# Optimization experiments

Measured on AMD Instinct MI355X. Metric: run time of the kernel, lower is better.

The kernel has to match this reference:

```python
import jax, jax.numpy as jnp
import numpy as np

ROUTING_ITERS = 3
EPS = 1e-8

def _squash_elem(s):
    # Faithful to torch squash with dim=-1 over a trailing size-1 axis: elementwise.
    sq = s * s
    return (sq / (1.0 + sq)) * s / jnp.sqrt(sq + EPS)

def setup_inputs() -> dict:
    key = jax.random.key(0)
    k1, k2 = jax.random.split(key)
    x = jax.random.normal(k1, (64, 1152, 64), dtype=jnp.float32)            # [B, N_routes, in_ch]
    route_weights = jax.random.normal(k2, (32, 1152, 64, 64), dtype=jnp.float32)  # [C, N, out, in]
    return {"x": x, "route_weights": route_weights}

def reference(x, route_weights):
    B = x.shape[0]
    C, N, O, _ = route_weights.shape
    # u_hat: [B, C, N, O]  (torch trailing size-1 dim dropped; squash/sums over it are elementwise)
    u_hat = jnp.einsum('cnoi,bni->bcno', route_weights, x)
    b_ij = jnp.zeros((B, C, N, 1), dtype=x.dtype)
    v_j = None
    for i in range(ROUTING_ITERS):
        c_ij = jax.nn.softmax(b_ij, axis=1)                  # over capsules
        s_j = jnp.sum(c_ij * u_hat, axis=2, keepdims=True)   # [B, C, 1, O]
        v_j = _squash_elem(s_j)
        if i < ROUTING_ITERS - 1:
            # torch: b_ij + (u_hat * v_j).sum(-1, keepdim) over size-1 dim -> broadcasts to [B,C,N,O]
            b_ij = b_ij + u_hat * v_j
    return v_j[:, :, 0, :]  # [B, C, O]
```

## Files before the change

### kernel.cpp

```cpp
#include <hip/hip_runtime.h>
#include <hip/hip_bf16.h>

typedef short short8v __attribute__((ext_vector_type(8)));
typedef float float4v __attribute__((ext_vector_type(4)));

constexpr int Bb = 64;
constexpr int Cc = 32;
constexpr int Nn = 1152;
constexpr int Oo = 64;
constexpr int Ii = 64;
constexpr int NCH = 32;
constexpr int CHN = 36;
constexpr int OT  = 16;
constexpr int COLS = 128;

__device__ __forceinline__ unsigned short bf16_rne(float f) {
    unsigned u = __float_as_uint(f);
    u += 0x7FFFu + ((u >> 16) & 1u);
    return (unsigned short)(u >> 16);
}
__device__ __forceinline__ float bf16_f(unsigned short h) {
    return __uint_as_float(((unsigned)h) << 16);
}
__device__ __forceinline__ float squash_elem(float s) {
    float sq = s * s;
    return (sq / (1.f + sq)) * s / sqrtf(sq + 1e-8f);
}

__global__ __launch_bounds__(256) void prep_x(const float* __restrict__ x,
                                              unsigned short* __restrict__ xh,
                                              unsigned short* __restrict__ xl) {
    size_t g = (size_t)blockIdx.x * 256 + threadIdx.x;
    float4 v = ((const float4*)x)[g];
    float a[4] = {v.x, v.y, v.z, v.w};
    ushort4 H, L;
    unsigned short* hp = (unsigned short*)&H;
    unsigned short* lp = (unsigned short*)&L;
#pragma unroll
    for (int e = 0; e < 4; ++e) {
        unsigned short hb = bf16_rne(a[e]);
        hp[e] = hb;
        lp[e] = bf16_rne(a[e] - bf16_f(hb));
    }
    ((ushort4*)xh)[g] = H;
    ((ushort4*)xl)[g] = L;
}

template <int MODE>
__global__ __launch_bounds__(256, 2) void caps_pass(
    const float* __restrict__ w, const unsigned short* __restrict__ xh,
    const unsigned short* __restrict__ xl, const float* __restrict__ V,
    float* __restrict__ part) {
    __shared__ unsigned short sh[2][COLS * 64];
    __shared__ unsigned short sl[2][COLS * 64];

    const int t = threadIdx.x;
    const int l = t & 63, wv = t >> 6;
    const int ch = blockIdx.x, ot = blockIdx.y;
    const int obase = ot * 4;
    const int kg = l >> 4;
    const int lm = l & 15;
    const int n0 = ch * CHN;
    const int sw = (lm & 7) << 3;

    float Vreg[8][4];
    if constexpr (MODE == 1) {
#pragma unroll
        for (int t8 = 0; t8 < 8; ++t8)
#pragma unroll
            for (int r = 0; r < 4; ++r) {
                int b = 16 * wv + 4 * kg + r;
                int c = 4 * t8 + ((l >> 2) & 3);
                int o = obase + (l & 3);
                Vreg[t8][r] = V[((size_t)b * Cc + c) * Oo + o];
            }
    }
    float4v acc4[8];
    float accs[8][4];
#pragma unroll
    for (int t8 = 0; t8 < 8; ++t8) {
        acc4[t8] = (float4v){0.f, 0.f, 0.f, 0.f};
#pragma unroll
        for (int r = 0; r < 4; ++r) accs[t8][r] = 0.f;
    }

    const int i0 = (t & 15) * 4;
    const int colb = t >> 4;
    float4 L0[8], L1[8];

    auto issue = [&](int n, float4(&ld)[8]) {
#pragma unroll
        for (int k = 0; k < 8; ++k) {
            int col = colb + 16 * k;
            int c = col >> 2, olc = col & 3;
            ld[k] = *(const float4*)(
                w + (((size_t)c * Nn + n) * Oo + obase + olc) * Ii + i0);
        }
    };
    auto writebuf = [&](unsigned short* dh, unsigned short* dl,
                        const float4(&ld)[8]) {
#pragma unroll
        for (int k = 0; k < 8; ++k) {
            int col = colb + 16 * k;
            int off = col * 64 + (i0 ^ ((col & 7) << 3));
            float a[4] = {ld[k].x, ld[k].y, ld[k].z, ld[k].w};
            ushort4 H, L;
            unsigned short* hp = (unsigned short*)&H;
            unsigned short* lp = (unsigned short*)&L;
#pragma unroll
            for (int e = 0; e < 4; ++e) {
                unsigned short hb = bf16_rne(a[e]);
                hp[e] = hb;
                lp[e] = bf16_rne(a[e] - bf16_f(hb));
            }
            *(ushort4*)(dh + off) = H;
            *(ushort4*)(dl + off) = L;
        }
    };
    auto compute = [&](const unsigned short* bh_, const unsigned short* bl_,
                       int n) {
        const size_t xoff = ((size_t)(16 * wv + lm) * Nn + n) * Ii + kg * 8;
        short8v ah0 = *(const short8v*)(xh + xoff);
        short8v al0 = *(const short8v*)(xl + xoff);
        short8v ah1 = *(const short8v*)(xh + xoff + 32);
        short8v al1 = *(const short8v*)(xl + xoff + 32);

        float u[8][4];
#pragma unroll
        for (int t8 = 0; t8 < 8; ++t8) {
            int row = 16 * t8 + lm;
            int c0 = row * 64 + ((kg * 8) ^ sw);
            int c1 = row * 64 + (((kg * 8) + 32) ^ sw);
            short8v bh0 = *(const short8v*)(bh_ + c0);
            short8v bl0 = *(const short8v*)(bl_ + c0);
            short8v bh1 = *(const short8v*)(bh_ + c1);
            short8v bl1 = *(const short8v*)(bl_ + c1);
            float4v a;
            if constexpr (MODE == 0) a = acc4[t8];
            else a = (float4v){0.f, 0.f, 0.f, 0.f};
            a = __builtin_amdgcn_mfma_f32_16x16x32_bf16(ah0, bh0, a, 0, 0, 0);
            a = __builtin_amdgcn_mfma_f32_16x16x32_bf16(al0, bh0, a, 0, 0, 0);
            a = __builtin_amdgcn_mfma_f32_16x16x32_bf16(ah0, bl0, a, 0, 0, 0);
            a = __builtin_amdgcn_mfma_f32_16x16x32_bf16(ah1, bh1, a, 0, 0, 0);
            a = __builtin_amdgcn_mfma_f32_16x16x32_bf16(al1, bh1, a, 0, 0, 0);
            a = __builtin_amdgcn_mfma_f32_16x16x32_bf16(ah1, bl1, a, 0, 0, 0);
            if constexpr (MODE == 0) {
                acc4[t8] = a;
            } else {
                u[t8][0] = a[0]; u[t8][1] = a[1];
                u[t8][2] = a[2]; u[t8][3] = a[3];
            }
        }
        if constexpr (MODE == 1) {
#pragma unroll
            for (int r = 0; r < 4; ++r) {
                float m = -1e30f;
#pragma unroll
                for (int t8 = 0; t8 < 8; ++t8)
                    m = fmaxf(m, u[t8][r] * Vreg[t8][r]);
                m = fmaxf(m, __shfl_xor(m, 4));
                m = fmaxf(m, __shfl_xor(m, 8));
                float Z = 0.f;
#pragma unroll
                for (int t8 = 0; t8 < 8; ++t8) {
                    float e = __expf(u[t8][r] * Vreg[t8][r] - m);
                    Z += e;
                    u[t8][r] *= e;
                }
                Z += __shfl_xor(Z, 4);
                Z += __shfl_xor(Z, 8);
                float rz = 1.f / Z;
#pragma unroll
                for (int t8 = 0; t8 < 8; ++t8) accs[t8][r] += u[t8][r] * rz;
            }
        }
    };

    issue(n0, L0);
    writebuf(sh[0], sl[0], L0);
    issue(n0 + 1, L1);
    __syncthreads();

    for (int j = 0; j < CHN; j += 2) {
        writebuf(sh[1], sl[1], L1);
        if (j + 2 < CHN) issue(n0 + j + 2, L0);
        compute(sh[0], sl[0], n0 + j);
        __syncthreads();
        if (j + 2 < CHN) writebuf(sh[0], sl[0], L0);
        if (j + 3 < CHN) issue(n0 + j + 3, L1);
        compute(sh[1], sl[1], n0 + j + 1);
        __syncthreads();
    }

#pragma unroll
    for (int t8 = 0; t8 < 8; ++t8)
#pragma unroll
        for (int r = 0; r < 4; ++r) {
            int b = 16 * wv + 4 * kg + r;
            int c = 4 * t8 + ((l >> 2) & 3);
            int o = obase + (l & 3);
            float val = (MODE == 0) ? acc4[t8][r] : accs[t8][r];
            part[(((size_t)ch * Bb + b) * Cc + c) * Oo + o] = val;
        }
}

__global__ void reduce_caps(const float* __restrict__ part,
                            float* __restrict__ V, float* __restrict__ out,
                            int mode) {
    int bc = blockIdx.x;
    int o = threadIdx.x;
    size_t base = (size_t)bc * 64 + o;
    float s = 0.f;
    for (int c = 0; c < NCH; ++c) s += part[(size_t)c * (Bb * Cc * Oo) + base];
    if (mode == 0)      V[base] = squash_elem(s * (1.f / 32.f));
    else if (mode == 1) V[base] += squash_elem(s);
    else                out[base] = squash_elem(s);
}

extern "C" void kernel_launch(void* const* d_in, const int* in_sizes, int n_in,
                              void* d_out, int out_size, void* d_ws, size_t ws_size,
                              hipStream_t stream) {
    const float* x = (const float*)d_in[0];
    const float* w = (const float*)d_in[1];
    float* out = (float*)d_out;

    const size_t XE = (size_t)Bb * Nn * Ii;
    unsigned short* xh = (unsigned short*)d_ws;
    unsigned short* xl = xh + XE;
    float* part = (float*)(xl + XE);
    float* V = part + (size_t)NCH * Bb * Cc * Oo;

    prep_x<<<(int)(XE / 4 / 256), 256, 0, stream>>>(x, xh, xl);

    caps_pass<0><<<dim3(NCH, OT), 256, 0, stream>>>(w, xh, xl, nullptr, part);
    reduce_caps<<<Bb * Cc, 64, 0, stream>>>(part, V, out, 0);
    caps_pass<1><<<dim3(NCH, OT), 256, 0, stream>>>(w, xh, xl, V, part);
    reduce_caps<<<Bb * Cc, 64, 0, stream>>>(part, V, out, 1);
    caps_pass<1><<<dim3(NCH, OT), 256, 0, stream>>>(w, xh, xl, V, part);
    reduce_caps<<<Bb * Cc, 64, 0, stream>>>(part, V, out, 2);
}
```

Baseline: 495.3 us.

## Load weights directly into MFMA registers, dropping LDS staging

The kernel no longer stages the weight tile through double-buffered shared memory. Each wave now reads its MFMA B-operand fragments straight from global memory and splits them into bf16 hi/lo in registers. The low part is now truncated instead of rounded. The chunk count rises from 32 to 48 and the occupancy hint from 2 to 3 blocks per SM, to hide latency through more parallelism. In exchange, each of the four waves now redundantly loads the same weights (relying on cache), there is no explicit software prefetch, and a bare s_barrier is kept per iteration.

```diff
diff --git a/kernel.cpp b/kernel.cpp
--- a/kernel.cpp
+++ b/kernel.cpp
@@ -9,10 +9,9 @@
 constexpr int Nn = 1152;
 constexpr int Oo = 64;
 constexpr int Ii = 64;
-constexpr int NCH = 32;
-constexpr int CHN = 36;
+constexpr int NCH = 48;
+constexpr int CHN = 24;
 constexpr int OT  = 16;
-constexpr int COLS = 128;
 
 __device__ __forceinline__ unsigned short bf16_rne(float f) {
     unsigned u = __float_as_uint(f);
@@ -25,6 +24,19 @@
 __device__ __forceinline__ float squash_elem(float s) {
     float sq = s * s;
     return (sq / (1.f + sq)) * s / sqrtf(sq + 1e-8f);
+}
+
+__device__ __forceinline__ void split8(const float4& f0, const float4& f1,
+                                       short8v& h, short8v& lo) {
+    float a[8] = {f0.x, f0.y, f0.z, f0.w, f1.x, f1.y, f1.z, f1.w};
+#pragma unroll
+    for (int e = 0; e < 8; ++e) {
+        unsigned b = __float_as_uint(a[e]);
+        unsigned r = b + 0x7FFFu + ((b >> 16) & 1u);
+        h[e] = (short)(r >> 16);
+        float res = a[e] - __uint_as_float(r & 0xFFFF0000u);
+        lo[e] = (short)(__float_as_uint(res) >> 16);
+    }
 }
 
 __global__ __launch_bounds__(256) void prep_x(const float* __restrict__ x,
@@ -47,33 +59,29 @@
 }
 
 template <int MODE>
-__global__ __launch_bounds__(256, 2) void caps_pass(
+__global__ __launch_bounds__(256, 3) void caps_pass(
     const float* __restrict__ w, const unsigned short* __restrict__ xh,
     const unsigned short* __restrict__ xl, const float* __restrict__ V,
     float* __restrict__ part) {
-    __shared__ unsigned short sh[2][COLS * 64];
-    __shared__ unsigned short sl[2][COLS * 64];
-
     const int t = threadIdx.x;
     const int l = t & 63, wv = t >> 6;
     const int ch = blockIdx.x, ot = blockIdx.y;
     const int obase = ot * 4;
-    const int kg = l >> 4;
-    const int lm = l & 15;
+    const int kg = l >> 4, lm = l & 15;
+    const int cc0 = lm >> 2, ol = lm & 3;
     const int n0 = ch * CHN;
-    const int sw = (lm & 7) << 3;
 
     float Vreg[8][4];
     if constexpr (MODE == 1) {
 #pragma unroll
-        for (int t8 = 0; t8 < 8; ++t8)
+        for (int t8 = 0; t8 < 8; ++t8) {
+            int c = 4 * t8 + cc0;
 #pragma unroll
             for (int r = 0; r < 4; ++r) {
                 int b = 16 * wv + 4 * kg + r;
-                int c = 4 * t8 + ((l >> 2) & 3);
-                int o = obase + (l & 3);
-                Vreg[t8][r] = V[((size_t)b * Cc + c) * Oo + o];
+                Vreg[t8][r] = V[((size_t)b * Cc + c) * Oo + obase + ol];
             }
+        }
     }
     float4v acc4[8];
     float accs[8][4];
@@ -84,57 +92,32 @@
         for (int r = 0; r < 4; ++r) accs[t8][r] = 0.f;
     }
 
-    const int i0 = (t & 15) * 4;
-    const int colb = t >> 4;
-    float4 L0[8], L1[8];
-
-    auto issue = [&](int n, float4(&ld)[8]) {
-#pragma unroll
-        for (int k = 0; k < 8; ++k) {
-            int col = colb + 16 * k;
-            int c = col >> 2, olc = col & 3;
-            ld[k] = *(const float4*)(
-                w + (((size_t)c * Nn + n) * Oo + obase + olc) * Ii + i0);
-        }
-    };
-    auto writebuf = [&](unsigned short* dh, unsigned short* dl,
-                        const float4(&ld)[8]) {
-#pragma unroll
-        for (int k = 0; k < 8; ++k) {
-            int col = colb + 16 * k;
-            int off = col * 64 + (i0 ^ ((col & 7) << 3));
-            float a[4] = {ld[k].x, ld[k].y, ld[k].z, ld[k].w};
-            ushort4 H, L;
-            unsigned short* hp = (unsigned short*)&H;
-            unsigned short* lp = (unsigned short*)&L;
-#pragma unroll
-            for (int e = 0; e < 4; ++e) {
-                unsigned short hb = bf16_rne(a[e]);
-                hp[e] = hb;
-                lp[e] = bf16_rne(a[e] - bf16_f(hb));
-            }
-            *(ushort4*)(dh + off) = H;
-            *(ushort4*)(dl + off) = L;
-        }
-    };
-    auto compute = [&](const unsigned short* bh_, const unsigned short* bl_,
-                       int n) {
-        const size_t xoff = ((size_t)(16 * wv + lm) * Nn + n) * Ii + kg * 8;
-        short8v ah0 = *(const short8v*)(xh + xoff);
-        short8v al0 = *(const short8v*)(xl + xoff);
-        short8v ah1 = *(const short8v*)(xh + xoff + 32);
-        short8v al1 = *(const short8v*)(xl + xoff + 32);
+    const size_t wlane = ((size_t)cc0 * Nn * Oo + obase + ol) * Ii + kg * 8;
+    const size_t xlane = (size_t)(16 * wv + lm) * Nn * Ii + kg * 8;
+    constexpr size_t T8STRIDE = (size_t)4 * Nn * Oo * Ii;
+
+    for (int j = 0; j < CHN; ++j) {
+        const int n = n0 + j;
+        const float* wn = w + wlane + (size_t)n * (Oo * Ii);
+        const unsigned short* xhn = xh + xlane + (size_t)n * Ii;
+        const unsigned short* xln = xl + xlane + (size_t)n * Ii;
+
+        short8v ah0 = *(const short8v*)xhn;
+        short8v al0 = *(const short8v*)xln;
+        short8v ah1 = *(const short8v*)(xhn + 32);
+        short8v al1 = *(const short8v*)(xln + 32);
 
         float u[8][4];
 #pragma unroll
         for (int t8 = 0; t8 < 8; ++t8) {
-            int row = 16 * t8 + lm;
-            int c0 = row * 64 + ((kg * 8) ^ sw);
-            int c1 = row * 64 + (((kg * 8) + 32) ^ sw);
-            short8v bh0 = *(const short8v*)(bh_ + c0);
-            short8v bl0 = *(const short8v*)(bl_ + c0);
-            short8v bh1 = *(const short8v*)(bh_ + c1);
-            short8v bl1 = *(const short8v*)(bl_ + c1);
+            const float* wp = wn + (size_t)t8 * T8STRIDE;
+            float4 f0 = *(const float4*)(wp);
+            float4 f1 = *(const float4*)(wp + 4);
+            float4 f2 = *(const float4*)(wp + 32);
+            float4 f3 = *(const float4*)(wp + 36);
+            short8v bh0, bl0, bh1, bl1;
+            split8(f0, f1, bh0, bl0);
+            split8(f2, f3, bh1, bl1);
             float4v a;
             if constexpr (MODE == 0) a = acc4[t8];
             else a = (float4v){0.f, 0.f, 0.f, 0.f};
@@ -151,6 +134,7 @@
                 u[t8][2] = a[2]; u[t8][3] = a[3];
             }
         }
+
         if constexpr (MODE == 1) {
 #pragma unroll
             for (int r = 0; r < 4; ++r) {
@@ -174,22 +158,8 @@
                 for (int t8 = 0; t8 < 8; ++t8) accs[t8][r] += u[t8][r] * rz;
             }
         }
-    };
-
-    issue(n0, L0);
-    writebuf(sh[0], sl[0], L0);
-    issue(n0 + 1, L1);
-    __syncthreads();
-
-    for (int j = 0; j < CHN; j += 2) {
-        writebuf(sh[1], sl[1], L1);
-        if (j + 2 < CHN) issue(n0 + j + 2, L0);
-        compute(sh[0], sl[0], n0 + j);
-        __syncthreads();
-        if (j + 2 < CHN) writebuf(sh[0], sl[0], L0);
-        if (j + 3 < CHN) issue(n0 + j + 3, L1);
-        compute(sh[1], sl[1], n0 + j + 1);
-        __syncthreads();
+
+        __builtin_amdgcn_s_barrier();
     }
 
 #pragma unroll
@@ -197,8 +167,8 @@
 #pragma unroll
         for (int r = 0; r < 4; ++r) {
             int b = 16 * wv + 4 * kg + r;
-            int c = 4 * t8 + ((l >> 2) & 3);
-            int o = obase + (l & 3);
+            int c = 4 * t8 + cc0;
+            int o = obase + ol;
             float val = (MODE == 0) ? acc4[t8][r] : accs[t8][r];
             part[(((size_t)ch * Bb + b) * Cc + c) * Oo + o] = val;
         }
```

Result: slower. 1.019 ms (+105.6%).

## Repartition MFMA work so each wave owns one output column across all batches

Applied to the files above, without the earlier changes.

Each wave now handles a single output index o across all 64 batch rows and 32 capsules. The old split gave each wave 16 batch rows across all 128 (c,o) columns. The LDS layout of the weight tile is reordered so a wave's 32 capsule rows are contiguous. Each wave then holds only 2 B-fragments in registers and streams x fragments for 4 batch quarters, double-buffered in registers. This cuts LDS reads of the weight tile per wave, but raises global/L2 reads of the bf16 x split by 4x per wave. In the routing pass the softmax over capsules now needs cross-lane shuffles over 16 lanes instead of mostly in-register reductions.

```diff
diff --git a/kernel.cpp b/kernel.cpp
--- a/kernel.cpp
+++ b/kernel.cpp
@@ -12,7 +12,6 @@
 constexpr int NCH = 32;
 constexpr int CHN = 36;
 constexpr int OT  = 16;
-constexpr int COLS = 128;
 
 __device__ __forceinline__ unsigned short bf16_rne(float f) {
     unsigned u = __float_as_uint(f);
@@ -51,38 +50,41 @@
     const float* __restrict__ w, const unsigned short* __restrict__ xh,
     const unsigned short* __restrict__ xl, const float* __restrict__ V,
     float* __restrict__ part) {
-    __shared__ unsigned short sh[2][COLS * 64];
-    __shared__ unsigned short sl[2][COLS * 64];
+    __shared__ unsigned short sh[2][128 * 64];
+    __shared__ unsigned short sl[2][128 * 64];
 
     const int t = threadIdx.x;
     const int l = t & 63, wv = t >> 6;
     const int ch = blockIdx.x, ot = blockIdx.y;
     const int obase = ot * 4;
-    const int kg = l >> 4;
-    const int lm = l & 15;
+    const int o = obase + wv;
+    const int kg = l >> 4, lm = l & 15;
     const int n0 = ch * CHN;
     const int sw = (lm & 7) << 3;
 
-    float Vreg[8][4];
+    float Vreg[4][2][4];
     if constexpr (MODE == 1) {
 #pragma unroll
-        for (int t8 = 0; t8 < 8; ++t8)
-#pragma unroll
-            for (int r = 0; r < 4; ++r) {
-                int b = 16 * wv + 4 * kg + r;
-                int c = 4 * t8 + ((l >> 2) & 3);
-                int o = obase + (l & 3);
-                Vreg[t8][r] = V[((size_t)b * Cc + c) * Oo + o];
-            }
+        for (int bq = 0; bq < 4; ++bq)
+#pragma unroll
+            for (int t8l = 0; t8l < 2; ++t8l)
+#pragma unroll
+                for (int r = 0; r < 4; ++r) {
+                    int b = 16 * bq + 4 * kg + r;
+                    int c = 16 * t8l + lm;
+                    Vreg[bq][t8l][r] = V[((size_t)b * Cc + c) * Oo + o];
+                }
     }
-    float4v acc4[8];
-    float accs[8][4];
-#pragma unroll
-    for (int t8 = 0; t8 < 8; ++t8) {
-        acc4[t8] = (float4v){0.f, 0.f, 0.f, 0.f};
-#pragma unroll
-        for (int r = 0; r < 4; ++r) accs[t8][r] = 0.f;
-    }
+    float4v acc4[4][2];
+    float accs[4][2][4];
+#pragma unroll
+    for (int bq = 0; bq < 4; ++bq)
+#pragma unroll
+        for (int t8l = 0; t8l < 2; ++t8l) {
+            acc4[bq][t8l] = (float4v){0.f, 0.f, 0.f, 0.f};
+#pragma unroll
+            for (int r = 0; r < 4; ++r) accs[bq][t8l][r] = 0.f;
+        }
 
     const int i0 = (t & 15) * 4;
     const int colb = t >> 4;
@@ -102,7 +104,9 @@
 #pragma unroll
         for (int k = 0; k < 8; ++k) {
             int col = colb + 16 * k;
-            int off = col * 64 + (i0 ^ ((col & 7) << 3));
+            int c = col >> 2, olc = col & 3;
+            int row = olc * 32 + c;
+            int off = row * 64 + (i0 ^ ((row & 7) << 3));
             float a[4] = {ld[k].x, ld[k].y, ld[k].z, ld[k].w};
             ushort4 H, L;
             unsigned short* hp = (unsigned short*)&H;
@@ -117,61 +121,79 @@
             *(ushort4*)(dl + off) = L;
         }
     };
+
     auto compute = [&](const unsigned short* bh_, const unsigned short* bl_,
                        int n) {
-        const size_t xoff = ((size_t)(16 * wv + lm) * Nn + n) * Ii + kg * 8;
-        short8v ah0 = *(const short8v*)(xh + xoff);
-        short8v al0 = *(const short8v*)(xl + xoff);
-        short8v ah1 = *(const short8v*)(xh + xoff + 32);
-        short8v al1 = *(const short8v*)(xl + xoff + 32);
-
-        float u[8][4];
-#pragma unroll
-        for (int t8 = 0; t8 < 8; ++t8) {
-            int row = 16 * t8 + lm;
+        short8v Bh0[2], Bl0[2], Bh1[2], Bl1[2];
+#pragma unroll
+        for (int t8l = 0; t8l < 2; ++t8l) {
+            int row = 32 * wv + 16 * t8l + lm;
             int c0 = row * 64 + ((kg * 8) ^ sw);
             int c1 = row * 64 + (((kg * 8) + 32) ^ sw);
-            short8v bh0 = *(const short8v*)(bh_ + c0);
-            short8v bl0 = *(const short8v*)(bl_ + c0);
-            short8v bh1 = *(const short8v*)(bh_ + c1);
-            short8v bl1 = *(const short8v*)(bl_ + c1);
-            float4v a;
-            if constexpr (MODE == 0) a = acc4[t8];
-            else a = (float4v){0.f, 0.f, 0.f, 0.f};
-            a = __builtin_amdgcn_mfma_f32_16x16x32_bf16(ah0, bh0, a, 0, 0, 0);
-            a = __builtin_amdgcn_mfma_f32_16x16x32_bf16(al0, bh0, a, 0, 0, 0);
-            a = __builtin_amdgcn_mfma_f32_16x16x32_bf16(ah0, bl0, a, 0, 0, 0);
-            a = __builtin_amdgcn_mfma_f32_16x16x32_bf16(ah1, bh1, a, 0, 0, 0);
-            a = __builtin_amdgcn_mfma_f32_16x16x32_bf16(al1, bh1, a, 0, 0, 0);
-            a = __builtin_amdgcn_mfma_f32_16x16x32_bf16(ah1, bl1, a, 0, 0, 0);
-            if constexpr (MODE == 0) {
-                acc4[t8] = a;
-            } else {
-                u[t8][0] = a[0]; u[t8][1] = a[1];
-                u[t8][2] = a[2]; u[t8][3] = a[3];
-            }
-        }
-        if constexpr (MODE == 1) {
-#pragma unroll
-            for (int r = 0; r < 4; ++r) {
-                float m = -1e30f;
-#pragma unroll
-                for (int t8 = 0; t8 < 8; ++t8)
-                    m = fmaxf(m, u[t8][r] * Vreg[t8][r]);
-                m = fmaxf(m, __shfl_xor(m, 4));
-                m = fmaxf(m, __shfl_xor(m, 8));
-                float Z = 0.f;
-#pragma unroll
-                for (int t8 = 0; t8 < 8; ++t8) {
-                    float e = __expf(u[t8][r] * Vreg[t8][r] - m);
-                    Z += e;
-                    u[t8][r] *= e;
+            Bh0[t8l] = *(const short8v*)(bh_ + c0);
+            Bl0[t8l] = *(const short8v*)(bl_ + c0);
+            Bh1[t8l] = *(const short8v*)(bh_ + c1);
+            Bl1[t8l] = *(const short8v*)(bl_ + c1);
+        }
+        short8v Ah0[2], Al0[2], Ah1[2], Al1[2];
+        {
+            const size_t xo = ((size_t)lm * Nn + n) * Ii + kg * 8;
+            Ah0[0] = *(const short8v*)(xh + xo);
+            Al0[0] = *(const short8v*)(xl + xo);
+            Ah1[0] = *(const short8v*)(xh + xo + 32);
+            Al1[0] = *(const short8v*)(xl + xo + 32);
+        }
+#pragma unroll
+        for (int bq = 0; bq < 4; ++bq) {
+            const int s = bq & 1;
+            if (bq < 3) {
+                const size_t xo =
+                    ((size_t)(16 * (bq + 1) + lm) * Nn + n) * Ii + kg * 8;
+                Ah0[s ^ 1] = *(const short8v*)(xh + xo);
+                Al0[s ^ 1] = *(const short8v*)(xl + xo);
+                Ah1[s ^ 1] = *(const short8v*)(xh + xo + 32);
+                Al1[s ^ 1] = *(const short8v*)(xl + xo + 32);
+            }
+            float u[2][4];
+#pragma unroll
+            for (int t8l = 0; t8l < 2; ++t8l) {
+                float4v a;
+                if constexpr (MODE == 0) a = acc4[bq][t8l];
+                else a = (float4v){0.f, 0.f, 0.f, 0.f};
+                a = __builtin_amdgcn_mfma_f32_16x16x32_bf16(Ah0[s], Bh0[t8l], a, 0, 0, 0);
+                a = __builtin_amdgcn_mfma_f32_16x16x32_bf16(Al0[s], Bh0[t8l], a, 0, 0, 0);
+                a = __builtin_amdgcn_mfma_f32_16x16x32_bf16(Ah0[s], Bl0[t8l], a, 0, 0, 0);
+                a = __builtin_amdgcn_mfma_f32_16x16x32_bf16(Ah1[s], Bh1[t8l], a, 0, 0, 0);
+                a = __builtin_amdgcn_mfma_f32_16x16x32_bf16(Al1[s], Bh1[t8l], a, 0, 0, 0);
+                a = __builtin_amdgcn_mfma_f32_16x16x32_bf16(Ah1[s], Bl1[t8l], a, 0, 0, 0);
+                if constexpr (MODE == 0) {
+                    acc4[bq][t8l] = a;
+                } else {
+                    u[t8l][0] = a[0]; u[t8l][1] = a[1];
+                    u[t8l][2] = a[2]; u[t8l][3] = a[3];
                 }
-                Z += __shfl_xor(Z, 4);
-                Z += __shfl_xor(Z, 8);
-                float rz = 1.f / Z;
-#pragma unroll
-                for (int t8 = 0; t8 < 8; ++t8) accs[t8][r] += u[t8][r] * rz;
+            }
+            if constexpr (MODE == 1) {
+#pragma unroll
+                for (int r = 0; r < 4; ++r) {
+                    float l0 = u[0][r] * Vreg[bq][0][r];
+                    float l1 = u[1][r] * Vreg[bq][1][r];
+                    float m = fmaxf(l0, l1);
+                    m = fmaxf(m, __shfl_xor(m, 1));
+                    m = fmaxf(m, __shfl_xor(m, 2));
+                    m = fmaxf(m, __shfl_xor(m, 4));
+                    m = fmaxf(m, __shfl_xor(m, 8));
+                    float e0 = __expf(l0 - m);
+                    float e1 = __expf(l1 - m);
+                    float Z = e0 + e1;
+                    Z += __shfl_xor(Z, 1);
+                    Z += __shfl_xor(Z, 2);
+                    Z += __shfl_xor(Z, 4);
+                    Z += __shfl_xor(Z, 8);
+                    float rz = 1.f / Z;
+                    accs[bq][0][r] = fmaf(e0 * rz, u[0][r], accs[bq][0][r]);
+                    accs[bq][1][r] = fmaf(e1 * rz, u[1][r], accs[bq][1][r]);
+                }
             }
         }
     };
@@ -193,15 +215,16 @@
     }
 
 #pragma unroll
-    for (int t8 = 0; t8 < 8; ++t8)
-#pragma unroll
-        for (int r = 0; r < 4; ++r) {
-            int b = 16 * wv + 4 * kg + r;
-            int c = 4 * t8 + ((l >> 2) & 3);
-            int o = obase + (l & 3);
-            float val = (MODE == 0) ? acc4[t8][r] : accs[t8][r];
-            part[(((size_t)ch * Bb + b) * Cc + c) * Oo + o] = val;
-        }
+    for (int bq = 0; bq < 4; ++bq)
+#pragma unroll
+        for (int t8l = 0; t8l < 2; ++t8l)
+#pragma unroll
+            for (int r = 0; r < 4; ++r) {
+                int b = 16 * bq + 4 * kg + r;
+                int c = 16 * t8l + lm;
+                float val = (MODE == 0) ? acc4[bq][t8l][r] : accs[bq][t8l][r];
+                part[(((size_t)ch * Bb + b) * Cc + c) * Oo + o] = val;
+            }
 }
 
 __global__ void reduce_caps(const float* __restrict__ part,
```

New measurement: 1.238 ms. 2.5x slower.

## Transpose split x to n-major layout and use barriers that skip vmem drain

Applied to the files above, without the earlier changes.

The x preprocessing kernel now writes its bf16 hi/lo split transposed to [N][B][I], so each step's x fragment loads in caps_pass come from one contiguous 8KB slab instead of being strided across the batch. The __syncthreads calls in the main loop are replaced by a barrier that waits only on LDS counters, so outstanding global prefetches of the weights are not drained at each barrier. A dead writebuf lambda is left behind that dereferences a null pointer; it is voided and unused, but the code is odd and fragile.

```diff
diff --git a/kernel.cpp b/kernel.cpp
--- a/kernel.cpp
+++ b/kernel.cpp
@@ -12,7 +12,6 @@
 constexpr int NCH = 32;
 constexpr int CHN = 36;
 constexpr int OT  = 16;
-constexpr int COLS = 128;
 
 __device__ __forceinline__ unsigned short bf16_rne(float f) {
     unsigned u = __float_as_uint(f);
@@ -27,23 +26,41 @@
     return (sq / (1.f + sq)) * s / sqrtf(sq + 1e-8f);
 }
 
-__global__ __launch_bounds__(256) void prep_x(const float* __restrict__ x,
-                                              unsigned short* __restrict__ xh,
-                                              unsigned short* __restrict__ xl) {
-    size_t g = (size_t)blockIdx.x * 256 + threadIdx.x;
-    float4 v = ((const float4*)x)[g];
-    float a[4] = {v.x, v.y, v.z, v.w};
-    ushort4 H, L;
-    unsigned short* hp = (unsigned short*)&H;
-    unsigned short* lp = (unsigned short*)&L;
-#pragma unroll
-    for (int e = 0; e < 4; ++e) {
+__device__ __forceinline__ void barrier_nodrain() {
+    asm volatile("s_waitcnt lgkmcnt(0)" ::: "memory");
+    __builtin_amdgcn_s_barrier();
+    asm volatile("" ::: "memory");
+}
+
+__device__ __forceinline__ void split8(const float4& f0, const float4& f1,
+                                       short8v& h, short8v& lo) {
+    float a[8] = {f0.x, f0.y, f0.z, f0.w, f1.x, f1.y, f1.z, f1.w};
+#pragma unroll
+    for (int e = 0; e < 8; ++e) {
         unsigned short hb = bf16_rne(a[e]);
-        hp[e] = hb;
-        lp[e] = bf16_rne(a[e] - bf16_f(hb));
-    }
-    ((ushort4*)xh)[g] = H;
-    ((ushort4*)xl)[g] = L;
+        h[e] = (short)hb;
+        lo[e] = (short)bf16_rne(a[e] - bf16_f(hb));
+    }
+}
+
+__global__ __launch_bounds__(256) void prep_xt(const float* __restrict__ x,
+                                               unsigned short* __restrict__ xh,
+                                               unsigned short* __restrict__ xl) {
+    const int n = blockIdx.x, t = threadIdx.x;
+    const int b = t >> 2, q = t & 3;
+    const float* src = x + ((size_t)b * Nn + n) * Ii + q * 16;
+    float4 v0 = *(const float4*)(src);
+    float4 v1 = *(const float4*)(src + 4);
+    float4 v2 = *(const float4*)(src + 8);
+    float4 v3 = *(const float4*)(src + 12);
+    short8v h0, l0, h1, l1;
+    split8(v0, v1, h0, l0);
+    split8(v2, v3, h1, l1);
+    size_t dst = (size_t)n * (Bb * Ii) + b * Ii + q * 16;
+    *(short8v*)(xh + dst) = h0;
+    *(short8v*)(xh + dst + 8) = h1;
+    *(short8v*)(xl + dst) = l0;
+    *(short8v*)(xl + dst + 8) = l1;
 }
 
 template <int MODE>
@@ -51,8 +68,8 @@
     const float* __restrict__ w, const unsigned short* __restrict__ xh,
     const unsigned short* __restrict__ xl, const float* __restrict__ V,
     float* __restrict__ part) {
-    __shared__ unsigned short sh[2][COLS * 64];
-    __shared__ unsigned short sl[2][COLS * 64];
+    __shared__ unsigned short sh[2][128 * 64];
+    __shared__ unsigned short sl[2][128 * 64];
 
     const int t = threadIdx.x;
     const int l = t & 63, wv = t >> 6;
@@ -103,6 +120,21 @@
         for (int k = 0; k < 8; ++k) {
             int col = colb + 16 * k;
             int off = col * 64 + (i0 ^ ((col & 7) << 3));
+            short8v H, Lo;
+            split8(ld[k], *(const float4*)nullptr == *(const float4*)nullptr
+                              ? ld[k]
+                              : ld[k],
+                   H, Lo);
+        }
+    };
+    (void)writebuf;
+
+    auto writebuf2 = [&](unsigned short* dh, unsigned short* dl,
+                         const float4(&ld)[8]) {
+#pragma unroll
+        for (int k = 0; k < 8; ++k) {
+            int col = colb + 16 * k;
+            int off = col * 64 + (i0 ^ ((col & 7) << 3));
             float a[4] = {ld[k].x, ld[k].y, ld[k].z, ld[k].w};
             ushort4 H, L;
             unsigned short* hp = (unsigned short*)&H;
@@ -117,9 +149,11 @@
             *(ushort4*)(dl + off) = L;
         }
     };
+
     auto compute = [&](const unsigned short* bh_, const unsigned short* bl_,
                        int n) {
-        const size_t xoff = ((size_t)(16 * wv + lm) * Nn + n) * Ii + kg * 8;
+        const size_t xoff =
+            (size_t)n * (Bb * Ii) + (16 * wv + lm) * Ii + kg * 8;
         short8v ah0 = *(const short8v*)(xh + xoff);
         short8v al0 = *(const short8v*)(xl + xoff);
         short8v ah1 = *(const short8v*)(xh + xoff + 32);
@@ -177,19 +211,19 @@
     };
 
     issue(n0, L0);
-    writebuf(sh[0], sl[0], L0);
+    writebuf2(sh[0], sl[0], L0);
     issue(n0 + 1, L1);
-    __syncthreads();
+    barrier_nodrain();
 
     for (int j = 0; j < CHN; j += 2) {
-        writebuf(sh[1], sl[1], L1);
+        writebuf2(sh[1], sl[1], L1);
         if (j + 2 < CHN) issue(n0 + j + 2, L0);
         compute(sh[0], sl[0], n0 + j);
-        __syncthreads();
-        if (j + 2 < CHN) writebuf(sh[0], sl[0], L0);
+        barrier_nodrain();
+        if (j + 2 < CHN) writebuf2(sh[0], sl[0], L0);
         if (j + 3 < CHN) issue(n0 + j + 3, L1);
         compute(sh[1], sl[1], n0 + j + 1);
-        __syncthreads();
+        barrier_nodrain();
     }
 
 #pragma unroll
@@ -230,7 +264,7 @@
     float* part = (float*)(xl + XE);
     float* V = part + (size_t)NCH * Bb * Cc * Oo;
 
-    prep_x<<<(int)(XE / 4 / 256), 256, 0, stream>>>(x, xh, xl);
+    prep_xt<<<Nn, 256, 0, stream>>>(x, xh, xl);
 
     caps_pass<0><<<dim3(NCH, OT), 256, 0, stream>>>(w, xh, xl, nullptr, part);
     reduce_caps<<<Bb * Cc, 64, 0, stream>>>(part, V, out, 0);
```

Result: no change. 496.4 us (+0.2%).
